# Optimization experiments

Measured on AMD Instinct MI355X. Metric: run time of the kernel, lower is better.

The kernel has to match this reference:

```python
import jax, jax.numpy as jnp
import numpy as np

S, L, K = 4, 256, 32          # num_states, seq length, neighbors
ORIG_H, EMB_H, EXV, RANK = 128, 256, 384, 16


def _integrate(x, Wq, Wk, seq_idx, emb_idx, hidden, rank):
    """AttentionIntegrator.forward: QK^T softmax -> double mean -> softmax -> weighted pool of raw x."""
    x = jnp.moveaxis(x, (seq_idx, emb_idx), (-2, -1))
    orig_shape = x.shape
    Ls = orig_shape[-2]
    xf = x.reshape(-1, Ls, hidden)               # (B, Ls, hidden)
    B = xf.shape[0]
    q = (xf @ Wq.T).reshape(B, Ls, rank, hidden)  # head_dim == hidden
    k = (xf @ Wk.T).reshape(B, Ls, rank, hidden)
    scale = 1.0 / jnp.sqrt(jnp.asarray(hidden, xf.dtype))
    scores = jnp.einsum('blhd,bmhd->bhlm', q, k) * scale
    attn = jax.nn.softmax(scores, axis=-1)        # (B, rank, Ls, Ls)
    w = jax.nn.softmax(attn.mean(axis=(1, 2)), axis=-1)  # (B, Ls)
    pooled = jnp.einsum('bl,bld->bd', w, xf)      # (B, hidden)
    return (pooled.reshape(*orig_shape[:-2], hidden),
            w.reshape(*orig_shape[:-2], Ls))


def setup_inputs() -> dict:
    key = jax.random.key(0)
    ks = jax.random.split(key, 12)
    sc = lambda fan_in: 1.0 / np.sqrt(fan_in)
    return {
        'h_V':    jax.random.normal(ks[0], (S, L, ORIG_H), jnp.float32),
        'h_EXV':  jax.random.normal(ks[1], (S, L, K, EXV), jnp.float32),
        'W_hV':   jax.random.normal(ks[2], (EMB_H, ORIG_H), jnp.float32) * sc(ORIG_H),
        'b_hV':   jnp.zeros((EMB_H,), jnp.float32),
        'Wq_hv':  jax.random.normal(ks[3], (RANK * EMB_H, EMB_H), jnp.float32) * sc(EMB_H),
        'Wk_hv':  jax.random.normal(ks[4], (RANK * EMB_H, EMB_H), jnp.float32) * sc(EMB_H),
        'Wq_ce':  jax.random.normal(ks[5], (RANK * EXV, EXV), jnp.float32) * sc(EXV),
        'Wk_ce':  jax.random.normal(ks[6], (RANK * EXV, EXV), jnp.float32) * sc(EXV),
        'W_ce':   jax.random.normal(ks[7], (EMB_H, EXV), jnp.float32) * sc(EXV),
        'b_ce':   jnp.zeros((EMB_H,), jnp.float32),
        'Wq_sce': jax.random.normal(ks[8], (RANK * EMB_H, EMB_H), jnp.float32) * sc(EMB_H),
        'Wk_sce': jax.random.normal(ks[9], (RANK * EMB_H, EMB_H), jnp.float32) * sc(EMB_H),
    }


def reference(h_V, h_EXV, W_hV, b_hV, Wq_hv, Wk_hv, Wq_ce, Wk_ce, W_ce, b_ce, Wq_sce, Wk_sce):
    # diffmodel.get_weights
    hv = h_V @ W_hV.T + b_hV                                  # (S, L, EMB_H)
    h_V_int, h_V_w = _integrate(hv, Wq_hv, Wk_hv, 0, 2, EMB_H, RANK)   # pool over states
    # chemical environment: pool over k neighbors per (state, position)
    ce, _local_w = _integrate(h_EXV, Wq_ce, Wk_ce, 2, 3, EXV, RANK)    # (S, L, EXV)
    ce = ce @ W_ce.T + b_ce                                   # (S, L, EMB_H)
    ce_int, ce_w = _integrate(ce, Wq_sce, Wk_sce, 0, 2, EMB_H, RANK)   # pool over states
    return (h_V_int[None], h_V_w[None], ce_int[None], ce_w[None])
```

## Files before the change

kernel.cpp:

```cpp
#include <hip/hip_runtime.h>

typedef _Float16 f16;
typedef _Float16 f16x8 __attribute__((ext_vector_type(8)));
typedef _Float16 f16x4 __attribute__((ext_vector_type(4)));
typedef float f32x4 __attribute__((ext_vector_type(4)));

#define MFMA16(a, b, c) __builtin_amdgcn_mfma_f32_16x16x32_f16(a, b, c, 0, 0, 0)
#define MFMA16K16(a, b, c) __builtin_amdgcn_mfma_f32_16x16x16f16(a, b, c, 0, 0, 0)

__global__ __launch_bounds__(256) void k_mt3(const float* __restrict__ Wq_hv,
                                             const float* __restrict__ Wk_hv,
                                             f16* __restrict__ mt_hv,
                                             const float* __restrict__ Wq_ce,
                                             const float* __restrict__ Wk_ce,
                                             f16* __restrict__ mt_ce,
                                             const float* __restrict__ Wq_sce,
                                             const float* __restrict__ Wk_sce,
                                             f16* __restrict__ mt_sce) {
    const int y = blockIdx.y;
    const float *Wq, *Wk;
    f16* MT;
    int H, ty;
    if (y < 16)      { Wq = Wq_hv;  Wk = Wk_hv;  MT = mt_hv;  H = 256; ty = y; }
    else if (y < 52) { Wq = Wq_ce;  Wk = Wk_ce;  MT = mt_ce;  H = 384; ty = y - 16; }
    else             { Wq = Wq_sce; Wk = Wk_sce; MT = mt_sce; H = 256; ty = y - 52; }

    const int h = blockIdx.x;
    const int ntile = H >> 6;
    const int nkk = H >> 5;
    const int frow = (ty / ntile) * 64;
    const int ecol = (ty % ntile) * 64;
    const int t = threadIdx.x;
    const int lane = t & 63;
    const int w = t >> 6;
    const int wr = w >> 1, wc = w & 1;

    __shared__ __align__(16) f16 As[64][40];
    __shared__ __align__(16) f16 Ks[64][40];

    f32x4 acc[2][2] = {};
    const int d = t >> 3;
    const int e8 = (t & 7) * 8;

    for (int kk = 0; kk < nkk; ++kk) {
        const float* gq = Wq + (size_t)(h * H + kk * 32 + d) * H + ecol + e8;
        const float* gk = Wk + (size_t)(h * H + kk * 32 + d) * H + frow + e8;
        float q[8], k[8];
#pragma unroll
        for (int i = 0; i < 8; ++i) { q[i] = gq[i]; k[i] = gk[i]; }
        __syncthreads();
#pragma unroll
        for (int i = 0; i < 8; ++i) { As[e8 + i][d] = (f16)q[i]; Ks[e8 + i][d] = (f16)k[i]; }
        __syncthreads();
        f16x8 a[2], b[2];
#pragma unroll
        for (int rt = 0; rt < 2; ++rt)
            a[rt] = *(const f16x8*)&Ks[wr * 32 + rt * 16 + (lane & 15)][(lane >> 4) * 8];
#pragma unroll
        for (int nt = 0; nt < 2; ++nt)
            b[nt] = *(const f16x8*)&As[wc * 32 + nt * 16 + (lane & 15)][(lane >> 4) * 8];
#pragma unroll
        for (int rt = 0; rt < 2; ++rt)
#pragma unroll
            for (int nt = 0; nt < 2; ++nt)
                acc[rt][nt] = MFMA16(a[rt], b[nt], acc[rt][nt]);
    }
#pragma unroll
    for (int rt = 0; rt < 2; ++rt)
#pragma unroll
        for (int nt = 0; nt < 2; ++nt)
#pragma unroll
            for (int j = 0; j < 4; ++j) {
                int f = frow + wr * 32 + rt * 16 + (lane >> 4) * 4 + j;
                int e = ecol + wc * 32 + nt * 16 + (lane & 15);
                MT[(((size_t)h * nkk + (e >> 5)) * H + f) * 32 + (e & 31)] = (f16)acc[rt][nt][j];
            }
}

__global__ __launch_bounds__(256) void k_lin(const float* __restrict__ in,
                                             const float* __restrict__ W,
                                             const float* __restrict__ bias,
                                             float* __restrict__ out, int K) {
    const int t = threadIdx.x;
    const int r0 = blockIdx.x * 4;
    __shared__ float ins[4][384];
    __shared__ float Ws[256][33];
#pragma unroll
    for (int r = 0; r < 4; ++r)
        for (int off = t; off < K; off += 256)
            ins[r][off] = in[(size_t)(r0 + r) * K + off];
    float acc[4] = {};
    for (int d0 = 0; d0 < K; d0 += 32) {
        __syncthreads();
        for (int i = t; i < 256 * 32; i += 256) {
            int j = i >> 5, dd = i & 31;
            Ws[j][dd] = W[(size_t)j * K + d0 + dd];
        }
        __syncthreads();
#pragma unroll 8
        for (int dd = 0; dd < 32; ++dd) {
            float wv = Ws[t][dd];
#pragma unroll
            for (int r = 0; r < 4; ++r) acc[r] += wv * ins[r][d0 + dd];
        }
    }
    float bv = bias[t];
#pragma unroll
    for (int r = 0; r < 4; ++r) out[(size_t)(r0 + r) * 256 + t] = acc[r] + bv;
}

__global__ __launch_bounds__(256) void k_small_int(const float* __restrict__ X,
                                                   const f16* __restrict__ MT,
                                                   float* __restrict__ wpart) {
    const int t = threadIdx.x;
    const int lane = t & 63;
    const int w = t >> 6;
    const int g = lane >> 4;
    const int l15 = lane & 15;
    const int pos0 = blockIdx.x * 8;
    const int h = blockIdx.y;

    __shared__ __align__(16) f16 Xs[32][264];
    __shared__ __align__(16) f16 Ts[32][264];

    {
        int row = t >> 3, d0 = (t & 7) * 32;
        int s = row & 3, p = row >> 2;
        const float* gx = X + (size_t)(s * 256 + pos0 + p) * 256 + d0;
#pragma unroll
        for (int i = 0; i < 32; i += 8) {
            float4 v0 = *(const float4*)(gx + i);
            float4 v1 = *(const float4*)(gx + i + 4);
            f16x8 o;
            o[0] = (f16)v0.x; o[1] = (f16)v0.y; o[2] = (f16)v0.z; o[3] = (f16)v0.w;
            o[4] = (f16)v1.x; o[5] = (f16)v1.y; o[6] = (f16)v1.z; o[7] = (f16)v1.w;
            *(f16x8*)&Xs[row][d0 + i] = o;
        }
    }
    __syncthreads();

    const f16* mh = MT + (size_t)h * 8 * 256 * 32;
    const int fb = w * 64 + l15;
    f32x4 acc[2][4] = {};
    f16x8 bq[4], bn[4];
#pragma unroll
    for (int nt = 0; nt < 4; ++nt)
        bq[nt] = *(const f16x8*)(mh + (size_t)(fb + nt * 16) * 32 + g * 8);
#pragma unroll
    for (int kk = 0; kk < 8; ++kk) {
        if (kk < 7) {
#pragma unroll
            for (int nt = 0; nt < 4; ++nt)
                bn[nt] = *(const f16x8*)(mh + ((size_t)(kk + 1) * 256 + fb + nt * 16) * 32 + g * 8);
        }
        f16x8 a[2];
#pragma unroll
        for (int mt = 0; mt < 2; ++mt)
            a[mt] = *(const f16x8*)&Xs[mt * 16 + l15][kk * 32 + g * 8];
#pragma unroll
        for (int mt = 0; mt < 2; ++mt)
#pragma unroll
            for (int nt = 0; nt < 4; ++nt)
                acc[mt][nt] = MFMA16(a[mt], bq[nt], acc[mt][nt]);
#pragma unroll
        for (int nt = 0; nt < 4; ++nt) bq[nt] = bn[nt];
    }
#pragma unroll
    for (int mt = 0; mt < 2; ++mt)
#pragma unroll
        for (int nt = 0; nt < 4; ++nt)
#pragma unroll
            for (int j = 0; j < 4; ++j)
                Ts[mt * 16 + g * 4 + j][w * 64 + nt * 16 + l15] = (f16)acc[mt][nt][j];
    __syncthreads();

    if (w < 2) {
        f32x4 sacc = {};
#pragma unroll
        for (int ks = 0; ks < 8; ++ks) {
            f16x8 a = *(const f16x8*)&Ts[w * 16 + l15][ks * 32 + g * 8];
            f16x8 b = *(const f16x8*)&Xs[w * 16 + l15][ks * 32 + g * 8];
            sacc = MFMA16(a, b, sacc);
        }
        if ((l15 >> 2) == g) {
            const float scale = 1.0f / 16.0f;
            float add = 0.f;
#pragma unroll
            for (int j = 0; j < 4; ++j) {
                float v = sacc[j] * scale;
                float m = v;
                m = fmaxf(m, __shfl_xor(m, 1));
                m = fmaxf(m, __shfl_xor(m, 2));
                float e = expf(v - m);
                float s2 = e;
                s2 += __shfl_xor(s2, 1);
                s2 += __shfl_xor(s2, 2);
                add += e / s2;
            }
            int pg = pos0 + w * 4 + g;
            wpart[((size_t)h * 256 + pg) * 4 + (l15 & 3)] = add;
        }
    }
}

__global__ __launch_bounds__(256) void k_small_fin(const float* __restrict__ wpart,
                                                   const float* __restrict__ X,
                                                   float* __restrict__ out_int,
                                                   float* __restrict__ out_w) {
    const int pos = blockIdx.x, t = threadIdx.x;
    __shared__ float red[64];
    __shared__ float ws[4];
    if (t < 64) red[t] = wpart[((size_t)(t >> 2) * 256 + pos) * 4 + (t & 3)];
    __syncthreads();
    if (t == 0) {
        float v[4];
#pragma unroll
        for (int s = 0; s < 4; ++s) {
            float x = 0.f;
            for (int hh = 0; hh < 16; ++hh) x += red[hh * 4 + s];
            v[s] = x * (1.0f / 64.0f);
        }
        float m = fmaxf(fmaxf(v[0], v[1]), fmaxf(v[2], v[3]));
        float sum = 0.f;
#pragma unroll
        for (int s = 0; s < 4; ++s) { v[s] = expf(v[s] - m); sum += v[s]; }
#pragma unroll
        for (int s = 0; s < 4; ++s) ws[s] = v[s] / sum;
    }
    __syncthreads();
    if (t < 4) out_w[pos * 4 + t] = ws[t];
    float v = 0.f;
#pragma unroll
    for (int s = 0; s < 4; ++s) v += ws[s] * X[(size_t)(s * 256 + pos) * 256 + t];
    out_int[(size_t)pos * 256 + t] = v;
}

#define BUF_OFF 98304

__global__ __launch_bounds__(512, 2) void k_ce_int(const float* __restrict__ Xg32,
                                                   const f16* __restrict__ MT,
                                                   float* __restrict__ acc_out) {
    const int t = threadIdx.x;
    const int lane = t & 63;
    const int w = t >> 6;
    const int g = lane >> 4;
    const int l15 = lane & 15;
    const int bg = blockIdx.x;

    extern __shared__ __align__(16) char smem[];
    char* BUF = smem + BUF_OFF;

    {
        const float* xg = Xg32 + (size_t)bg * 128 * 384;
#pragma unroll
        for (int p = 0; p < 12; ++p) {
            int idx = p * 512 + t;
            int row = idx / 48, s = idx - row * 48;
            int c = s ^ (row & 7);
            const float* src = xg + row * 384 + c * 8;
            float4 v0 = *(const float4*)src;
            float4 v1 = *(const float4*)(src + 4);
            f16x8 o;
            o[0] = (f16)v0.x; o[1] = (f16)v0.y; o[2] = (f16)v0.z; o[3] = (f16)v0.w;
            o[4] = (f16)v1.x; o[5] = (f16)v1.y; o[6] = (f16)v1.z; o[7] = (f16)v1.w;
            *(f16x8*)(smem + idx * 16) = o;
        }
    }
    __syncthreads();

    const f16* mall = MT;
    const int frow = w * 48 + l15;

    f16x8 A[3][3];
#pragma unroll
    for (int ft = 0; ft < 3; ++ft) {
        A[0][ft] = *(const f16x8*)(mall + (size_t)(frow + ft * 16) * 32 + g * 8);
        A[1][ft] = *(const f16x8*)(mall + (size_t)12288 + (size_t)(frow + ft * 16) * 32 + g * 8);
    }

    for (int hi = 0; hi < 16; ++hi) {
        f32x4 acc[3][8] = {};
#pragma unroll
        for (int kk = 0; kk < 12; ++kk) {
            {
                int step = hi * 12 + kk + 2;
                int ns = step < 192 ? step : 191;
#pragma unroll
                for (int ft = 0; ft < 3; ++ft)
                    A[(kk + 2) % 3][ft] =
                        *(const f16x8*)(mall + (size_t)ns * 12288 + (size_t)(frow + ft * 16) * 32 + g * 8);
            }
            f16x8 xb[8];
#pragma unroll
            for (int mt = 0; mt < 8; ++mt) {
                int row = mt * 16 + l15;
                int ch = kk * 4 + g;
                xb[mt] = *(const f16x8*)(smem + row * 768 + ((ch ^ (row & 7)) << 4));
            }
            __builtin_amdgcn_s_setprio(1);
#pragma unroll
            for (int ft = 0; ft < 3; ++ft)
#pragma unroll
                for (int mt = 0; mt < 8; ++mt)
                    acc[ft][mt] = MFMA16(A[kk % 3][ft], xb[mt], acc[ft][mt]);
            __builtin_amdgcn_s_setprio(0);
        }

        f16x4 bf[3][8];
#pragma unroll
        for (int ft = 0; ft < 3; ++ft)
#pragma unroll
            for (int mt = 0; mt < 8; ++mt) {
                f32x4 v = acc[ft][mt];
                f16x4 o;
                o[0] = (f16)v[0]; o[1] = (f16)v[1]; o[2] = (f16)v[2]; o[3] = (f16)v[3];
                bf[ft][mt] = o;
            }

#pragma unroll
        for (int r = 0; r < 2; ++r) {
            f32x4 s2[2][2][2] = {};
#pragma unroll
            for (int bb = 0; bb < 2; ++bb) {
                const int b = 2 * r + bb;
#pragma unroll
                for (int ks = 0; ks < 3; ++ks)
#pragma unroll
                    for (int it = 0; it < 2; ++it) {
                        int row = b * 32 + it * 16 + l15;
                        int ch = 6 * w + 2 * ks + (g >> 1);
                        f16x4 av = *(const f16x4*)(smem + row * 768 +
                                                   ((ch ^ (row & 7)) << 4) + 8 * (g & 1));
#pragma unroll
                        for (int lt = 0; lt < 2; ++lt)
                            s2[bb][it][lt] = MFMA16K16(av, bf[ks][2 * b + lt], s2[bb][it][lt]);
                    }
            }
#pragma unroll
            for (int bb = 0; bb < 2; ++bb)
#pragma unroll
                for (int it = 0; it < 2; ++it)
#pragma unroll
                    for (int lt = 0; lt < 2; ++lt)
                        *(f32x4*)(BUF + w * 8192 + (bb * 4 + it * 2 + lt) * 1024 + lane * 16) =
                            s2[bb][it][lt];
            __syncthreads();

            if ((w >> 2) == r) {
                const int wl = w & 3;
                const int bb = wl >> 1;
                const int it = wl & 1;
                const int b = 2 * r + bb;
                f32x4 sum0 = {0.f, 0.f, 0.f, 0.f};
                f32x4 sum1 = {0.f, 0.f, 0.f, 0.f};
#pragma unroll
                for (int src = 0; src < 8; ++src) {
                    const char* pb = BUF + src * 8192 + (bb * 4 + it * 2) * 1024 + lane * 16;
                    sum0 += *(const f32x4*)pb;
                    sum1 += *(const f32x4*)(pb + 1024);
                }
                const float scale = 0.051031036307982884f;
                float cs0 = 0.f, cs1 = 0.f;
#pragma unroll
                for (int j = 0; j < 4; ++j) {
                    float v0 = sum0[j] * scale, v1 = sum1[j] * scale;
                    float m = fmaxf(v0, v1);
                    m = fmaxf(m, __shfl_xor(m, 1));
                    m = fmaxf(m, __shfl_xor(m, 2));
                    m = fmaxf(m, __shfl_xor(m, 4));
                    m = fmaxf(m, __shfl_xor(m, 8));
                    float e0 = expf(v0 - m), e1 = expf(v1 - m);
                    float s = e0 + e1;
                    s += __shfl_xor(s, 1);
                    s += __shfl_xor(s, 2);
                    s += __shfl_xor(s, 4);
                    s += __shfl_xor(s, 8);
                    float inv = 1.f / s;
                    cs0 += e0 * inv;
                    cs1 += e1 * inv;
                }
                cs0 += __shfl_xor(cs0, 16); cs0 += __shfl_xor(cs0, 32);
                cs1 += __shfl_xor(cs1, 16); cs1 += __shfl_xor(cs1, 32);
                if (lane < 16) {
                    float* o = acc_out + (((size_t)hi * 1024 + bg * 4 + b) * 2 + it) * 32;
                    o[l15] = cs0;
                    o[16 + l15] = cs1;
                }
            }
            __syncthreads();
        }
    }
}

__global__ __launch_bounds__(256) void k_ce_pool(const float* __restrict__ accp,
                                                 const float* __restrict__ exv,
                                                 float* __restrict__ pooled) {
    const int b = blockIdx.x;
    const int t = threadIdx.x;
    __shared__ float ww[32];
    if (t < 32) {
        float s = 0.f;
#pragma unroll
        for (int h = 0; h < 16; ++h) {
            s += accp[(((size_t)h * 1024 + b) * 2 + 0) * 32 + t];
            s += accp[(((size_t)h * 1024 + b) * 2 + 1) * 32 + t];
        }
        s *= (1.0f / 512.0f);
        float m = s;
        m = fmaxf(m, __shfl_xor(m, 1));
        m = fmaxf(m, __shfl_xor(m, 2));
        m = fmaxf(m, __shfl_xor(m, 4));
        m = fmaxf(m, __shfl_xor(m, 8));
        m = fmaxf(m, __shfl_xor(m, 16));
        float e = __expf(s - m);
        float sum = e;
        sum += __shfl_xor(sum, 1);
        sum += __shfl_xor(sum, 2);
        sum += __shfl_xor(sum, 4);
        sum += __shfl_xor(sum, 8);
        sum += __shfl_xor(sum, 16);
        ww[t] = e / sum;
    }
    __syncthreads();
    for (int d = t; d < 384; d += 256) {
        float v = 0.f;
#pragma unroll
        for (int m = 0; m < 32; ++m) v += ww[m] * exv[((size_t)b * 32 + m) * 384 + d];
        pooled[(size_t)b * 384 + d] = v;
    }
}

extern "C" void kernel_launch(void* const* d_in, const int* in_sizes, int n_in,
                              void* d_out, int out_size, void* d_ws, size_t ws_size,
                              hipStream_t stream) {
    const float* h_V    = (const float*)d_in[0];
    const float* h_EXV  = (const float*)d_in[1];
    const float* W_hV   = (const float*)d_in[2];
    const float* b_hV   = (const float*)d_in[3];
    const float* Wq_hv  = (const float*)d_in[4];
    const float* Wk_hv  = (const float*)d_in[5];
    const float* Wq_ce  = (const float*)d_in[6];
    const float* Wk_ce  = (const float*)d_in[7];
    const float* W_ce   = (const float*)d_in[8];
    const float* b_ce   = (const float*)d_in[9];
    const float* Wq_sce = (const float*)d_in[10];
    const float* Wk_sce = (const float*)d_in[11];
    float* out = (float*)d_out;

    char* ws = (char*)d_ws;
    f16*   mt_hv  = (f16*)(ws + 0);
    f16*   mt_sce = (f16*)(ws + 2097152);
    f16*   mt_ce  = (f16*)(ws + 4194304);
    float* hv     = (float*)(ws + 8912896);
    float* ce     = (float*)(ws + 9961472);
    float* accp   = (float*)(ws + 11010048);
    float* pooled = (float*)(ws + 15204352);
    float* wpart  = accp;

    k_mt3<<<dim3(16, 68), 256, 0, stream>>>(Wq_hv, Wk_hv, mt_hv,
                                            Wq_ce, Wk_ce, mt_ce,
                                            Wq_sce, Wk_sce, mt_sce);
    k_lin<<<256, 256, 0, stream>>>(h_V, W_hV, b_hV, hv, 128);
    k_small_int<<<dim3(32, 16), 256, 0, stream>>>(hv, mt_hv, wpart);
    k_small_fin<<<256, 256, 0, stream>>>(wpart, hv, out + 0, out + 65536);
    k_ce_int<<<dim3(256), 512, 163840, stream>>>(h_EXV, mt_ce, accp);
    k_ce_pool<<<1024, 256, 0, stream>>>(accp, h_EXV, pooled);
    k_lin<<<256, 256, 0, stream>>>(pooled, W_ce, b_ce, ce, 384);
    k_small_int<<<dim3(32, 16), 256, 0, stream>>>(ce, mt_sce, wpart);
    k_small_fin<<<256, 256, 0, stream>>>(wpart, ce, out + 66560, out + 132096);
}
```

Measured before the change: 300.9 us.

## Restructure ce attention kernel: one head per wave, smaller blocks, no cross-wave reduction

Rewrites the chemical-environment integrator kernel so each wave owns one attention head, looping over 12 feature chunks and accumulating the score tiles in registers. The previous scheme split the feature dimension across waves and reduced partial scores through shared memory with block barriers. Each block now covers 2 batches (64 rows) instead of 4, which halves the LDS footprint and doubles the grid to 512 blocks. Exp is switched to the fast intrinsic. In exchange, each wave reloads more of the weight matrix per row handled and does less reuse per MFMA, and the fast exp gives up some accuracy.

```diff
diff --git a/kernel.cpp b/kernel.cpp
--- a/kernel.cpp
+++ b/kernel.cpp
@@ -235,11 +235,9 @@
     out_int[(size_t)pos * 256 + t] = v;
 }
 
-#define BUF_OFF 98304
-
-__global__ __launch_bounds__(512, 2) void k_ce_int(const float* __restrict__ Xg32,
-                                                   const f16* __restrict__ MT,
-                                                   float* __restrict__ acc_out) {
+__global__ __launch_bounds__(512) void k_ce_int(const float* __restrict__ Xg32,
+                                                const f16* __restrict__ MT,
+                                                float* __restrict__ acc_out) {
     const int t = threadIdx.x;
     const int lane = t & 63;
     const int w = t >> 6;
@@ -248,12 +246,11 @@
     const int bg = blockIdx.x;
 
     extern __shared__ __align__(16) char smem[];
-    char* BUF = smem + BUF_OFF;
 
     {
-        const float* xg = Xg32 + (size_t)bg * 128 * 384;
-#pragma unroll
-        for (int p = 0; p < 12; ++p) {
+        const float* xg = Xg32 + (size_t)bg * 64 * 384;
+#pragma unroll
+        for (int p = 0; p < 6; ++p) {
             int idx = p * 512 + t;
             int row = idx / 48, s = idx - row * 48;
             int c = s ^ (row & 7);
@@ -268,98 +265,83 @@
     }
     __syncthreads();
 
-    const f16* mall = MT;
-    const int frow = w * 48 + l15;
-
-    f16x8 A[3][3];
-#pragma unroll
-    for (int ft = 0; ft < 3; ++ft) {
-        A[0][ft] = *(const f16x8*)(mall + (size_t)(frow + ft * 16) * 32 + g * 8);
-        A[1][ft] = *(const f16x8*)(mall + (size_t)12288 + (size_t)(frow + ft * 16) * 32 + g * 8);
-    }
-
-    for (int hi = 0; hi < 16; ++hi) {
-        f32x4 acc[3][8] = {};
-#pragma unroll
-        for (int kk = 0; kk < 12; ++kk) {
-            {
-                int step = hi * 12 + kk + 2;
-                int ns = step < 192 ? step : 191;
-#pragma unroll
-                for (int ft = 0; ft < 3; ++ft)
-                    A[(kk + 2) % 3][ft] =
-                        *(const f16x8*)(mall + (size_t)ns * 12288 + (size_t)(frow + ft * 16) * 32 + g * 8);
+    const float scale = 0.051031036307982884f;
+
+    for (int h2 = 0; h2 < 2; ++h2) {
+        const int h = h2 * 8 + w;
+        const f16* mh = MT + (size_t)h * 12 * 12288;
+
+        f32x4 S2[2][2][2] = {};
+
+        f16x8 A[2][2];
+#pragma unroll
+        for (int ft = 0; ft < 2; ++ft)
+            A[0][ft] = *(const f16x8*)(mh + (size_t)(0 * 32 + ft * 16 + l15) * 32 + g * 8);
+
+        for (int c = 0; c < 12; ++c) {
+            f32x4 acc[2][4] = {};
+#pragma unroll
+            for (int kk = 0; kk < 12; ++kk) {
+                const int step = c * 12 + kk;
+                {
+                    int ns = step + 1;
+                    int nc = ns / 12, nk = ns - nc * 12;
+                    if (nc > 11) { nc = 11; nk = 11; }
+#pragma unroll
+                    for (int ft = 0; ft < 2; ++ft)
+                        A[(step + 1) & 1][ft] =
+                            *(const f16x8*)(mh + (size_t)nk * 12288 +
+                                            (size_t)(nc * 32 + ft * 16 + l15) * 32 + g * 8);
+                }
+                f16x8 xb[4];
+#pragma unroll
+                for (int mt = 0; mt < 4; ++mt) {
+                    int row = mt * 16 + l15;
+                    int ch = kk * 4 + g;
+                    xb[mt] = *(const f16x8*)(smem + row * 768 + ((ch ^ (row & 7)) << 4));
+                }
+                __builtin_amdgcn_s_setprio(1);
+#pragma unroll
+                for (int ft = 0; ft < 2; ++ft)
+#pragma unroll
+                    for (int mt = 0; mt < 4; ++mt)
+                        acc[ft][mt] = MFMA16(A[step & 1][ft], xb[mt], acc[ft][mt]);
+                __builtin_amdgcn_s_setprio(0);
             }
-            f16x8 xb[8];
-#pragma unroll
-            for (int mt = 0; mt < 8; ++mt) {
-                int row = mt * 16 + l15;
-                int ch = kk * 4 + g;
-                xb[mt] = *(const f16x8*)(smem + row * 768 + ((ch ^ (row & 7)) << 4));
-            }
-            __builtin_amdgcn_s_setprio(1);
-#pragma unroll
-            for (int ft = 0; ft < 3; ++ft)
-#pragma unroll
-                for (int mt = 0; mt < 8; ++mt)
-                    acc[ft][mt] = MFMA16(A[kk % 3][ft], xb[mt], acc[ft][mt]);
-            __builtin_amdgcn_s_setprio(0);
-        }
-
-        f16x4 bf[3][8];
-#pragma unroll
-        for (int ft = 0; ft < 3; ++ft)
-#pragma unroll
-            for (int mt = 0; mt < 8; ++mt) {
-                f32x4 v = acc[ft][mt];
-                f16x4 o;
-                o[0] = (f16)v[0]; o[1] = (f16)v[1]; o[2] = (f16)v[2]; o[3] = (f16)v[3];
-                bf[ft][mt] = o;
-            }
-
-#pragma unroll
-        for (int r = 0; r < 2; ++r) {
-            f32x4 s2[2][2][2] = {};
-#pragma unroll
-            for (int bb = 0; bb < 2; ++bb) {
-                const int b = 2 * r + bb;
-#pragma unroll
-                for (int ks = 0; ks < 3; ++ks)
+
+            f16x4 bf[2][4];
+#pragma unroll
+            for (int ft = 0; ft < 2; ++ft)
+#pragma unroll
+                for (int mt = 0; mt < 4; ++mt) {
+                    f32x4 v = acc[ft][mt];
+                    f16x4 o;
+                    o[0] = (f16)v[0]; o[1] = (f16)v[1]; o[2] = (f16)v[2]; o[3] = (f16)v[3];
+                    bf[ft][mt] = o;
+                }
+
+#pragma unroll
+            for (int b = 0; b < 2; ++b)
+#pragma unroll
+                for (int ks = 0; ks < 2; ++ks)
 #pragma unroll
                     for (int it = 0; it < 2; ++it) {
                         int row = b * 32 + it * 16 + l15;
-                        int ch = 6 * w + 2 * ks + (g >> 1);
+                        int ch = c * 4 + ks * 2 + (g >> 1);
                         f16x4 av = *(const f16x4*)(smem + row * 768 +
                                                    ((ch ^ (row & 7)) << 4) + 8 * (g & 1));
 #pragma unroll
                         for (int lt = 0; lt < 2; ++lt)
-                            s2[bb][it][lt] = MFMA16K16(av, bf[ks][2 * b + lt], s2[bb][it][lt]);
+                            S2[b][it][lt] = MFMA16K16(av, bf[ks][2 * b + lt], S2[b][it][lt]);
                     }
-            }
-#pragma unroll
-            for (int bb = 0; bb < 2; ++bb)
-#pragma unroll
-                for (int it = 0; it < 2; ++it)
-#pragma unroll
-                    for (int lt = 0; lt < 2; ++lt)
-                        *(f32x4*)(BUF + w * 8192 + (bb * 4 + it * 2 + lt) * 1024 + lane * 16) =
-                            s2[bb][it][lt];
-            __syncthreads();
-
-            if ((w >> 2) == r) {
-                const int wl = w & 3;
-                const int bb = wl >> 1;
-                const int it = wl & 1;
-                const int b = 2 * r + bb;
-                f32x4 sum0 = {0.f, 0.f, 0.f, 0.f};
-                f32x4 sum1 = {0.f, 0.f, 0.f, 0.f};
-#pragma unroll
-                for (int src = 0; src < 8; ++src) {
-                    const char* pb = BUF + src * 8192 + (bb * 4 + it * 2) * 1024 + lane * 16;
-                    sum0 += *(const f32x4*)pb;
-                    sum1 += *(const f32x4*)(pb + 1024);
-                }
-                const float scale = 0.051031036307982884f;
+        }
+
+#pragma unroll
+        for (int b = 0; b < 2; ++b)
+#pragma unroll
+            for (int it = 0; it < 2; ++it) {
+                f32x4 sum0 = S2[b][it][0];
+                f32x4 sum1 = S2[b][it][1];
                 float cs0 = 0.f, cs1 = 0.f;
 #pragma unroll
                 for (int j = 0; j < 4; ++j) {
@@ -369,7 +351,7 @@
                     m = fmaxf(m, __shfl_xor(m, 2));
                     m = fmaxf(m, __shfl_xor(m, 4));
                     m = fmaxf(m, __shfl_xor(m, 8));
-                    float e0 = expf(v0 - m), e1 = expf(v1 - m);
+                    float e0 = __expf(v0 - m), e1 = __expf(v1 - m);
                     float s = e0 + e1;
                     s += __shfl_xor(s, 1);
                     s += __shfl_xor(s, 2);
@@ -382,13 +364,11 @@
                 cs0 += __shfl_xor(cs0, 16); cs0 += __shfl_xor(cs0, 32);
                 cs1 += __shfl_xor(cs1, 16); cs1 += __shfl_xor(cs1, 32);
                 if (lane < 16) {
-                    float* o = acc_out + (((size_t)hi * 1024 + bg * 4 + b) * 2 + it) * 32;
+                    float* o = acc_out + (((size_t)h * 1024 + bg * 2 + b) * 2 + it) * 32;
                     o[l15] = cs0;
                     o[16 + l15] = cs1;
                 }
             }
-            __syncthreads();
-        }
     }
 }
 
@@ -463,7 +443,7 @@
     k_lin<<<256, 256, 0, stream>>>(h_V, W_hV, b_hV, hv, 128);
     k_small_int<<<dim3(32, 16), 256, 0, stream>>>(hv, mt_hv, wpart);
     k_small_fin<<<256, 256, 0, stream>>>(wpart, hv, out + 0, out + 65536);
-    k_ce_int<<<dim3(256), 512, 163840, stream>>>(h_EXV, mt_ce, accp);
+    k_ce_int<<<dim3(512), 512, 49152, stream>>>(h_EXV, mt_ce, accp);
     k_ce_pool<<<1024, 256, 0, stream>>>(accp, h_EXV, pooled);
     k_lin<<<256, 256, 0, stream>>>(pooled, W_ce, b_ce, ce, 384);
     k_small_int<<<dim3(32, 16), 256, 0, stream>>>(ce, mt_sce, wpart);
```

After: 304.3 us. Within noise of the previous version (+1.1%).
